# Kernel tuning notes

Measured on AMD Instinct MI355X. Metric: run time of the kernel, lower is better.

Reference implementation:

```python
import jax, jax.numpy as jnp
import numpy as np

N_TOKENS = 4096
EMBED = 2048
D_ATTN = 2048


def setup_inputs() -> dict:
    key = jax.random.key(0)
    k1, k2, k3, k4 = jax.random.split(key, 4)
    # torch.rand -> uniform [0,1); keeps scores positive so the multiplicative
    # -inf mask acts as a clean causal mask (faithful to original behavior).
    token_embeddings = jax.random.uniform(k1, (N_TOKENS, EMBED), dtype=jnp.float32)
    W_Q = jax.random.uniform(k2, (EMBED, D_ATTN), dtype=jnp.float32)
    W_K = jax.random.uniform(k3, (EMBED, D_ATTN), dtype=jnp.float32)
    W_V = jax.random.uniform(k4, (EMBED, D_ATTN), dtype=jnp.float32)
    return {"token_embeddings": token_embeddings, "W_Q": W_Q, "W_K": W_K, "W_V": W_V}


def reference(token_embeddings, W_Q, W_K, W_V):
    n = token_embeddings.shape[0]
    d = W_Q.shape[1]
    # mask: 1 on/below diagonal, -inf strictly above (multiplicative, as in source)
    neg_inf = jnp.float32(-jnp.inf)
    mask = jnp.tril(jnp.ones((n, n), dtype=jnp.float32)) + jnp.triu(
        jnp.full((n, n), neg_inf, dtype=jnp.float32), k=1
    )
    Q = token_embeddings @ W_Q          # (n, d)
    K = token_embeddings @ W_K          # (n, d)
    V = token_embeddings @ W_V          # (n, d)
    scores = (Q @ K.T) * mask           # (n, n); upper tri -> -inf (scores > 0)
    scores = scores / jnp.sqrt(jnp.float32(d))
    attn = jax.nn.softmax(scores, axis=-1)
    return attn @ V                     # (n, d)
```

## Files before the change

### kernel.cpp

```cpp
#include <hip/hip_runtime.h>
#include <hip/hip_bf16.h>
#include <cstdint>
#include <cstddef>
#include <cmath>

#define N_TOK 4096
#define EMB   2048
#define DATT  2048

typedef __attribute__((ext_vector_type(8))) short short8;
typedef __attribute__((ext_vector_type(4))) short shortx4;
typedef __attribute__((ext_vector_type(4))) float f32x4;

#define MFMA(a, b, c) __builtin_amdgcn_mfma_f32_16x16x32_bf16(a, b, c, 0, 0, 0)

__device__ __forceinline__ short f2bs(float f) {
  __hip_bfloat16 h = __float2bfloat16(f);
  return __builtin_bit_cast(short, h);
}
__device__ __forceinline__ float bs2f(short s) {
  return __uint_as_float(((unsigned)(unsigned short)s) << 16);
}
__device__ __forceinline__ float ldin(const void* p, size_t i, int isbf) {
  if (isbf) {
    unsigned short u = ((const unsigned short*)p)[i];
    return __uint_as_float(((unsigned int)u) << 16);
  }
  return ((const float*)p)[i];
}

__device__ __forceinline__ size_t swz(int r, int c, int kdim) {
  return ((size_t)((r >> 7) * (kdim >> 3) + (c >> 3)) << 10) +
         (size_t)((r & 127) << 3) + (c & 7);
}

__device__ __forceinline__ void gl16(const short* g, short* l) {
  __builtin_amdgcn_global_load_lds(
      (const __attribute__((address_space(1))) unsigned int*)(const void*)g,
      (__attribute__((address_space(3))) unsigned int*)(void*)l, 16, 0, 0);
}

template <bool THREE>
__device__ __forceinline__ void gemm_core(const short* Ah, const short* Al,
                                          const short* Bh, const short* Bl,
                                          int chunks, int apan, int bpan,
                                          int kmax, short* lds,
                                          f32x4 acc[4][4]) {
  const int NSL = THREE ? 4 : 2;
  int tid = threadIdx.x;
  int lane = tid & 63;
  int wave = tid >> 6;
  int ln = lane & 15, quad = lane >> 4;
  int wm = (wave >> 1) * 64, wn = (wave & 1) * 64;
  int wofs = wave * 512;

  auto stage = [&](int b, int k0) {
    size_t ao = ((size_t)(apan * chunks + (k0 >> 3))) << 10;
    size_t bo = ((size_t)(bpan * chunks + (k0 >> 3))) << 10;
    short* base = lds + b * NSL * 4096;
    const short* sa = Ah + ao + tid * 8;
    const short* sb = Bh + bo + tid * 8;
    gl16(sa,        base + wofs);
    gl16(sa + 2048, base + wofs + 2048);
    gl16(sb,        base + 4096 + wofs);
    gl16(sb + 2048, base + 4096 + wofs + 2048);
    if (THREE) {
      const short* sal = Al + ao + tid * 8;
      const short* sbl = Bl + bo + tid * 8;
      gl16(sal,        base + 8192 + wofs);
      gl16(sal + 2048, base + 8192 + wofs + 2048);
      gl16(sbl,        base + 12288 + wofs);
      gl16(sbl + 2048, base + 12288 + wofs + 2048);
    }
  };

  stage(0, 0);
  int cur = 0;
  int abase = quad * 1024 + (wm + ln) * 8;
  int bbase = quad * 1024 + (wn + ln) * 8;
  for (int k0 = 0; k0 < kmax; k0 += 32) {
    __syncthreads();
    if (k0 + 32 < kmax) stage(cur ^ 1, k0 + 32);
    const short* B0 = lds + cur * NSL * 4096;
    short8 fah[4], fbh[4];
#pragma unroll
    for (int i = 0; i < 4; ++i) fah[i] = *(const short8*)(B0 + abase + i * 128);
#pragma unroll
    for (int j = 0; j < 4; ++j) fbh[j] = *(const short8*)(B0 + 4096 + bbase + j * 128);
    if (THREE) {
      short8 fal[4], fbl[4];
#pragma unroll
      for (int i = 0; i < 4; ++i) fal[i] = *(const short8*)(B0 + 8192 + abase + i * 128);
#pragma unroll
      for (int j = 0; j < 4; ++j) fbl[j] = *(const short8*)(B0 + 12288 + bbase + j * 128);
#pragma unroll
      for (int j = 0; j < 4; ++j)
#pragma unroll
        for (int i = 0; i < 4; ++i) {
          acc[i][j] = MFMA(fah[i], fbh[j], acc[i][j]);
          acc[i][j] = MFMA(fah[i], fbl[j], acc[i][j]);
          acc[i][j] = MFMA(fal[i], fbh[j], acc[i][j]);
        }
    } else {
#pragma unroll
      for (int j = 0; j < 4; ++j)
#pragma unroll
        for (int i = 0; i < 4; ++i) acc[i][j] = MFMA(fah[i], fbh[j], acc[i][j]);
    }
    cur ^= 1;
  }
}

__global__ void k_sniff(const void* x, int* flag) {
  if (threadIdx.x == 0 && blockIdx.x == 0) {
    const unsigned short* u = (const unsigned short*)x;
    int bf = 1;
    for (int i = 0; i < 256; ++i) {
      unsigned short v = u[i];
      if ((v & 0x8000u) || ((v & 0x7FFFu) >= 0x3F80u)) { bf = 0; break; }
    }
    *flag = bf;
  }
}

__global__ __launch_bounds__(256) void k_xbar(const void* X, float* xbar,
                                              const int* flagp) {
  int isbf = *flagp;
  int e = blockIdx.x * 256 + threadIdx.x;
  float s = 0.f;
  for (int r = 0; r < 256; ++r) s += ldin(X, (size_t)r * EMB + e, isbf);
  xbar[e] = s * (1.f / 256.f);
}

__global__ __launch_bounds__(256) void k_split_x(const void* X, short* Xh, short* Xl,
                                                 const int* flagp) {
  int isbf = *flagp;
  size_t base = ((size_t)blockIdx.x * 256 + threadIdx.x) * 4;
  int r = (int)(base >> 11), c = (int)(base & 2047);
  shortx4 h, l;
#pragma unroll
  for (int u = 0; u < 4; ++u) {
    float x = ldin(X, base + u, isbf);
    short hh = f2bs(x);
    h[u] = hh;
    l[u] = f2bs(x - bs2f(hh));
  }
  size_t o = swz(r, c, EMB);
  *(shortx4*)(Xh + o) = h;
  *(shortx4*)(Xl + o) = l;
}

__global__ __launch_bounds__(256) void k_transpose_split(const void* W, short* Wth,
                                                         short* Wtl, int R, int C,
                                                         const int* flagp, int wlo) {
  __shared__ float T[64][65];
  int isbf = *flagp;
  int r0 = blockIdx.y * 64, c0 = blockIdx.x * 64;
  int tid = threadIdx.x;
#pragma unroll
  for (int it = 0; it < 16; ++it) {
    int idx = tid + it * 256;
    int row = idx >> 6, col = idx & 63;
    T[row][col] = ldin(W, (size_t)(r0 + row) * C + c0 + col, isbf);
  }
  __syncthreads();
#pragma unroll
  for (int it = 0; it < 16; ++it) {
    int idx = tid + it * 256;
    int row = idx >> 6, col = idx & 63;
    float x = T[col][row];
    short h = f2bs(x);
    size_t o = swz(c0 + row, r0 + col, R);
    Wth[o] = h;
    if (wlo) Wtl[o] = f2bs(x - bs2f(h));
  }
}

__global__ __launch_bounds__(256) void k_kbar(const short* Wth, const short* Wtl,
                                              const float* xbar, float* kbar) {
  int d = blockIdx.x;
  float s = 0.f;
  for (int e = threadIdx.x; e < EMB; e += 256) {
    size_t o = swz(d, e, EMB);
    s += xbar[e] * (bs2f(Wth[o]) + bs2f(Wtl[o]));
  }
  __shared__ float red[4];
#pragma unroll
  for (int off = 32; off > 0; off >>= 1) s += __shfl_down(s, off);
  if ((threadIdx.x & 63) == 0) red[threadIdx.x >> 6] = s;
  __syncthreads();
  if (threadIdx.x == 0) kbar[d] = red[0] + red[1] + red[2] + red[3];
}

__global__ __launch_bounds__(256, 2) void k_proj3(const short* Ah, const short* Al,
                                                  const short* Bh, const short* Bl,
                                                  short* Ch, short* Cl,
                                                  const float* bias) {
  __shared__ short lds[2 * 4 * 4096];
  f32x4 acc[4][4] = {};
  int row0 = blockIdx.y * 128, col0 = blockIdx.x * 128;
  gemm_core<true>(Ah, Al, Bh, Bl, EMB >> 3, row0 >> 7, col0 >> 7, EMB, lds, acc);
  int tid = threadIdx.x;
  int wave = tid >> 6, lane = tid & 63;
  int ln = lane & 15, quad = lane >> 4;
  int wm = (wave >> 1) * 64, wn = (wave & 1) * 64;
#pragma unroll
  for (int i = 0; i < 4; ++i)
#pragma unroll
    for (int j = 0; j < 4; ++j)
#pragma unroll
      for (int r = 0; r < 4; ++r) {
        int row = row0 + wm + i * 16 + quad * 4 + r;
        int col = col0 + wn + j * 16 + ln;
        float x = acc[i][j][r];
        if (bias) x -= bias[col];
        short h = f2bs(x);
        size_t o = swz(row, col, DATT);
        Ch[o] = h;
        Cl[o] = f2bs(x - bs2f(h));
      }
}

__global__ __launch_bounds__(256, 2) void k_proj1(const short* Ah, const short* Bh,
                                                  short* Ch) {
  __shared__ short lds[2 * 2 * 4096];
  f32x4 acc[4][4] = {};
  int row0 = blockIdx.y * 128, col0 = blockIdx.x * 128;
  gemm_core<false>(Ah, nullptr, Bh, nullptr, EMB >> 3, row0 >> 7, col0 >> 7, EMB,
                   lds, acc);
  int tid = threadIdx.x;
  int wave = tid >> 6, lane = tid & 63;
  int ln = lane & 15, quad = lane >> 4;
  int wm = (wave >> 1) * 64, wn = (wave & 1) * 64;
#pragma unroll
  for (int i = 0; i < 4; ++i)
#pragma unroll
    for (int j = 0; j < 4; ++j)
#pragma unroll
      for (int r = 0; r < 4; ++r) {
        int row = row0 + wm + i * 16 + quad * 4 + r;
        int col = col0 + wn + j * 16 + ln;
        Ch[swz(row, col, N_TOK)] = f2bs(acc[i][j][r]);
      }
}

__global__ __launch_bounds__(256, 2) void k_score3(const short* Qh, const short* Ql,
                                                   const short* Kh, const short* Kl,
                                                   float* S) {
  int bi = blockIdx.x;
  int by = (int)((sqrtf(8.f * (float)bi + 1.f) - 1.f) * 0.5f);
  while ((by + 1) * (by + 2) / 2 <= bi) ++by;
  while (by * (by + 1) / 2 > bi) --by;
  int bx = bi - by * (by + 1) / 2;
  __shared__ short lds[2 * 4 * 4096];
  f32x4 acc[4][4] = {};
  gemm_core<true>(Qh, Ql, Kh, Kl, DATT >> 3, by, bx, DATT, lds, acc);
  int row0 = by * 128, col0 = bx * 128;
  int tid = threadIdx.x;
  int wave = tid >> 6, lane = tid & 63;
  int ln = lane & 15, quad = lane >> 4;
  int wm = (wave >> 1) * 64, wn = (wave & 1) * 64;
  const float scale = 0.022097086912079608f;
#pragma unroll
  for (int i = 0; i < 4; ++i)
#pragma unroll
    for (int j = 0; j < 4; ++j)
#pragma unroll
      for (int r = 0; r < 4; ++r) {
        int row = row0 + wm + i * 16 + quad * 4 + r;
        int col = col0 + wn + j * 16 + ln;
        if (col <= row) S[(size_t)row * N_TOK + col] = acc[i][j][r] * scale;
      }
}

__global__ __launch_bounds__(256) void k_softmax(const float* S, short* P) {
  int i = blockIdx.x;
  const float* row = S + (size_t)i * N_TOK;
  int len = i + 1;
  int tid = threadIdx.x;
  __shared__ float red[4];
  float m = -3.402823466e38f;
  for (int j = tid; j < len; j += 256) m = fmaxf(m, row[j]);
#pragma unroll
  for (int off = 32; off > 0; off >>= 1) m = fmaxf(m, __shfl_down(m, off));
  if ((tid & 63) == 0) red[tid >> 6] = m;
  __syncthreads();
  m = fmaxf(fmaxf(red[0], red[1]), fmaxf(red[2], red[3]));
  __syncthreads();
  float s = 0.f;
  for (int j = tid; j < len; j += 256) s += __expf(row[j] - m);
#pragma unroll
  for (int off = 32; off > 0; off >>= 1) s += __shfl_down(s, off);
  if ((tid & 63) == 0) red[tid >> 6] = s;
  __syncthreads();
  s = red[0] + red[1] + red[2] + red[3];
  float inv = 1.f / s;
  size_t rbase = ((size_t)(i >> 7) * (N_TOK >> 3) << 10) + (size_t)((i & 127) << 3);
  for (int j = tid; j < len; j += 256)
    P[rbase + ((size_t)(j >> 3) << 10) + (j & 7)] = f2bs(__expf(row[j] - m) * inv);
  for (int j = len + tid; j < N_TOK; j += 256)
    P[rbase + ((size_t)(j >> 3) << 10) + (j & 7)] = 0;
}

__global__ __launch_bounds__(256, 2) void k_out(const short* Ph, const short* Vh,
                                                void* Co, const int* flagp) {
  __shared__ short lds[2 * 2 * 4096];
  f32x4 acc[4][4] = {};
  int row0 = blockIdx.y * 128, col0 = blockIdx.x * 128;
  gemm_core<false>(Ph, nullptr, Vh, nullptr, N_TOK >> 3, row0 >> 7, col0 >> 7,
                   row0 + 128, lds, acc);
  int isbf = *flagp;
  int tid = threadIdx.x;
  int wave = tid >> 6, lane = tid & 63;
  int ln = lane & 15, quad = lane >> 4;
  int wm = (wave >> 1) * 64, wn = (wave & 1) * 64;
#pragma unroll
  for (int i = 0; i < 4; ++i)
#pragma unroll
    for (int j = 0; j < 4; ++j)
#pragma unroll
      for (int r = 0; r < 4; ++r) {
        int row = row0 + wm + i * 16 + quad * 4 + r;
        int col = col0 + wn + j * 16 + ln;
        size_t idx = (size_t)row * DATT + col;
        if (isbf) ((__hip_bfloat16*)Co)[idx] = __float2bfloat16(acc[i][j][r]);
        else      ((float*)Co)[idx] = acc[i][j][r];
      }
}

extern "C" void kernel_launch(void* const* d_in, const int* in_sizes, int n_in,
                              void* d_out, int out_size, void* d_ws, size_t ws_size,
                              hipStream_t stream) {
  const void* X  = d_in[0];
  const void* WQ = d_in[1];
  const void* WK = d_in[2];
  const void* WV = d_in[3];

  float* ws   = (float*)d_ws;
  int*   flag = (int*)d_ws;
  float* xbar = ws + 256;
  float* kbar = ws + 2560;
  short* p0   = (short*)(ws + 16384);
  const size_t M8 = (size_t)N_TOK * DATT;
  const size_t M4 = (size_t)EMB * DATT;
  short* Xh  = p0;
  short* Xl  = Xh + M8;
  short* Wth = Xl + M8;
  short* Wtl = Wth + M4;
  float* S   = (float*)p0;
  short* Qh  = p0 + 4 * M8;
  short* Ql  = Qh + M8;
  short* Kh  = Ql + M8;
  short* Kl  = Kh + M8;
  short* Vt  = Kl + M8;
  short* P   = Qh;

  dim3 blk(256);

  k_sniff<<<1, 64, 0, stream>>>(X, flag);
  k_xbar<<<EMB / 256, blk, 0, stream>>>(X, xbar, flag);
  k_split_x<<<(N_TOK * EMB) / 1024, blk, 0, stream>>>(X, Xh, Xl, flag);

  dim3 gt(DATT / 64, EMB / 64);
  dim3 gq(DATT / 128, N_TOK / 128);
  dim3 gv(N_TOK / 128, DATT / 128);

  k_transpose_split<<<gt, blk, 0, stream>>>(WQ, Wth, Wtl, EMB, DATT, flag, 1);
  k_proj3<<<gq, blk, 0, stream>>>(Xh, Xl, Wth, Wtl, Qh, Ql, nullptr);
  k_transpose_split<<<gt, blk, 0, stream>>>(WK, Wth, Wtl, EMB, DATT, flag, 1);
  k_kbar<<<DATT, blk, 0, stream>>>(Wth, Wtl, xbar, kbar);
  k_proj3<<<gq, blk, 0, stream>>>(Xh, Xl, Wth, Wtl, Kh, Kl, kbar);
  k_transpose_split<<<gt, blk, 0, stream>>>(WV, Wth, nullptr, EMB, DATT, flag, 0);
  k_proj1<<<gv, blk, 0, stream>>>(Wth, Xh, Vt);

  dim3 gs((N_TOK / 128) * (N_TOK / 128 + 1) / 2);
  k_score3<<<gs, blk, 0, stream>>>(Qh, Ql, Kh, Kl, S);

  k_softmax<<<N_TOK, blk, 0, stream>>>(S, P);

  dim3 go(DATT / 128, N_TOK / 128);
  k_out<<<go, blk, 0, stream>>>(P, Vt, d_out, flag);
}
```

Before: 700.1 us.

## Use 256x128 tiles with 512 threads and triple-buffered interleaved prefetch GEMM

Adds a new GEMM core, gemm256, used by the Q/K/V projection and output kernels. Each block now runs 8 waves on a 256x128 output tile, with a three-stage LDS ring filled by direct global-to-LDS loads. Prefetches for the stage two steps ahead are issued between the MFMA sub-blocks, and raised wave priority and explicit waitcnt/barrier scheduling are meant to keep the matrix units busy and hide load latency. In exchange, LDS use per block is much larger (about 147KB for the three-product path), so only one block fits per CU, and the grid has half as many blocks.

```diff
diff --git a/kernel.cpp b/kernel.cpp
--- a/kernel.cpp
+++ b/kernel.cpp
@@ -38,6 +38,180 @@
   __builtin_amdgcn_global_load_lds(
       (const __attribute__((address_space(1))) unsigned int*)(const void*)g,
       (__attribute__((address_space(3))) unsigned int*)(void*)l, 16, 0, 0);
+}
+
+template <bool THREE>
+__device__ __forceinline__ void gemm256(const short* __restrict__ Ah,
+                                        const short* __restrict__ Al,
+                                        const short* __restrict__ Bh,
+                                        const short* __restrict__ Bl,
+                                        int kch, int apan, int bpan, int kmax,
+                                        short* lds, f32x4 acc[4][4]) {
+  const int BUF = THREE ? 24576 : 12288;
+  const int ALS = 8192;
+  const int BHS = THREE ? 16384 : 8192;
+  const int BLS = 20480;
+  int tid = threadIdx.x;
+  int lane = tid & 63, wave = tid >> 6;
+  int ln = lane & 15, quad = lane >> 4;
+  int wm = (wave >> 1) * 64, wn = (wave & 1) * 64;
+  int nt = kmax >> 5;
+  int aoffs = ((wm & 128) ? 4096 : 0) + quad * 1024 + ((wm & 64) + ln) * 8;
+  int boffs = quad * 1024 + (wn + ln) * 8;
+
+  auto stg = [&](const short* g, short* l) {
+    gl16(g + tid * 8, l + wave * 512);
+  };
+  const size_t kstr = (size_t)kch << 10;
+
+  auto stageAll = [&](int b, int s) {
+    short* Pb = lds + b * BUF;
+    size_t a0 = ((size_t)(apan * kch + (s << 2)) << 10);
+    size_t b0 = ((size_t)(bpan * kch + (s << 2)) << 10);
+    stg(Ah + a0, Pb);
+    stg(Ah + a0 + kstr, Pb + 4096);
+    if (THREE) {
+      stg(Al + a0, Pb + ALS);
+      stg(Al + a0 + kstr, Pb + ALS + 4096);
+    }
+    stg(Bh + b0, Pb + BHS);
+    if (THREE) stg(Bl + b0, Pb + BLS);
+  };
+  stageAll(0, 0);
+  stageAll(1, 1);
+
+  int bi = 0;
+  for (int t = 0; t < nt; ++t) {
+    if (t + 1 < nt) {
+      if constexpr (THREE) asm volatile("s_waitcnt vmcnt(6)" ::: "memory");
+      else                 asm volatile("s_waitcnt vmcnt(3)" ::: "memory");
+    } else {
+      asm volatile("s_waitcnt vmcnt(0)" ::: "memory");
+    }
+    __builtin_amdgcn_s_barrier();
+    __builtin_amdgcn_sched_barrier(0);
+
+    short* L = lds + bi * BUF;
+    int pi = bi + 2; if (pi > 2) pi -= 3;
+    short* Pb = lds + pi * BUF;
+    bool pf = (t + 2 < nt);
+    size_t pa0 = ((size_t)(apan * kch + ((t + 2) << 2)) << 10);
+    size_t pb0 = ((size_t)(bpan * kch + ((t + 2) << 2)) << 10);
+
+    short8 bh[4];
+#pragma unroll
+    for (int j = 0; j < 4; ++j)
+      bh[j] = *(const short8*)(L + BHS + boffs + j * 128);
+
+    if constexpr (THREE) {
+      short8 bl[4];
+#pragma unroll
+      for (int j = 0; j < 4; ++j)
+        bl[j] = *(const short8*)(L + BLS + boffs + j * 128);
+      {
+        short8 ah = *(const short8*)(L + aoffs);
+        short8 al = *(const short8*)(L + ALS + aoffs);
+        if (pf) { stg(Ah + pa0, Pb); stg(Ah + pa0 + kstr, Pb + 4096); }
+        __builtin_amdgcn_s_barrier();
+        asm volatile("s_waitcnt lgkmcnt(0)" ::: "memory");
+        __builtin_amdgcn_sched_barrier(0);
+        __builtin_amdgcn_s_setprio(1);
+#pragma unroll
+        for (int j = 0; j < 4; ++j) {
+          acc[0][j] = MFMA(ah, bh[j], acc[0][j]);
+          acc[0][j] = MFMA(ah, bl[j], acc[0][j]);
+          acc[0][j] = MFMA(al, bh[j], acc[0][j]);
+        }
+        __builtin_amdgcn_s_setprio(0);
+        __builtin_amdgcn_s_barrier();
+      }
+      {
+        short8 ah = *(const short8*)(L + aoffs + 128);
+        short8 al = *(const short8*)(L + ALS + aoffs + 128);
+        if (pf) { stg(Al + pa0, Pb + ALS); stg(Al + pa0 + kstr, Pb + ALS + 4096); }
+        __builtin_amdgcn_s_barrier();
+        asm volatile("s_waitcnt lgkmcnt(0)" ::: "memory");
+        __builtin_amdgcn_sched_barrier(0);
+        __builtin_amdgcn_s_setprio(1);
+#pragma unroll
+        for (int j = 0; j < 4; ++j) {
+          acc[1][j] = MFMA(ah, bh[j], acc[1][j]);
+          acc[1][j] = MFMA(ah, bl[j], acc[1][j]);
+          acc[1][j] = MFMA(al, bh[j], acc[1][j]);
+        }
+        __builtin_amdgcn_s_setprio(0);
+        __builtin_amdgcn_s_barrier();
+      }
+      {
+        short8 ah = *(const short8*)(L + aoffs + 256);
+        short8 al = *(const short8*)(L + ALS + aoffs + 256);
+        if (pf) stg(Bh + pb0, Pb + BHS);
+        __builtin_amdgcn_s_barrier();
+        asm volatile("s_waitcnt lgkmcnt(0)" ::: "memory");
+        __builtin_amdgcn_sched_barrier(0);
+        __builtin_amdgcn_s_setprio(1);
+#pragma unroll
+        for (int j = 0; j < 4; ++j) {
+          acc[2][j] = MFMA(ah, bh[j], acc[2][j]);
+          acc[2][j] = MFMA(ah, bl[j], acc[2][j]);
+          acc[2][j] = MFMA(al, bh[j], acc[2][j]);
+        }
+        __builtin_amdgcn_s_setprio(0);
+        __builtin_amdgcn_s_barrier();
+      }
+      {
+        short8 ah = *(const short8*)(L + aoffs + 384);
+        short8 al = *(const short8*)(L + ALS + aoffs + 384);
+        if (pf) stg(Bl + pb0, Pb + BLS);
+        __builtin_amdgcn_s_barrier();
+        asm volatile("s_waitcnt lgkmcnt(0)" ::: "memory");
+        __builtin_amdgcn_sched_barrier(0);
+        __builtin_amdgcn_s_setprio(1);
+#pragma unroll
+        for (int j = 0; j < 4; ++j) {
+          acc[3][j] = MFMA(ah, bh[j], acc[3][j]);
+          acc[3][j] = MFMA(ah, bl[j], acc[3][j]);
+          acc[3][j] = MFMA(al, bh[j], acc[3][j]);
+        }
+        __builtin_amdgcn_s_setprio(0);
+        __builtin_amdgcn_s_barrier();
+      }
+    } else {
+      {
+        short8 a0 = *(const short8*)(L + aoffs);
+        short8 a1 = *(const short8*)(L + aoffs + 128);
+        if (pf) { stg(Ah + pa0, Pb); stg(Ah + pa0 + kstr, Pb + 4096); }
+        __builtin_amdgcn_s_barrier();
+        asm volatile("s_waitcnt lgkmcnt(0)" ::: "memory");
+        __builtin_amdgcn_sched_barrier(0);
+        __builtin_amdgcn_s_setprio(1);
+#pragma unroll
+        for (int j = 0; j < 4; ++j) {
+          acc[0][j] = MFMA(a0, bh[j], acc[0][j]);
+          acc[1][j] = MFMA(a1, bh[j], acc[1][j]);
+        }
+        __builtin_amdgcn_s_setprio(0);
+        __builtin_amdgcn_s_barrier();
+      }
+      {
+        short8 a2 = *(const short8*)(L + aoffs + 256);
+        short8 a3 = *(const short8*)(L + aoffs + 384);
+        if (pf) stg(Bh + pb0, Pb + BHS);
+        __builtin_amdgcn_s_barrier();
+        asm volatile("s_waitcnt lgkmcnt(0)" ::: "memory");
+        __builtin_amdgcn_sched_barrier(0);
+        __builtin_amdgcn_s_setprio(1);
+#pragma unroll
+        for (int j = 0; j < 4; ++j) {
+          acc[2][j] = MFMA(a2, bh[j], acc[2][j]);
+          acc[3][j] = MFMA(a3, bh[j], acc[3][j]);
+        }
+        __builtin_amdgcn_s_setprio(0);
+        __builtin_amdgcn_s_barrier();
+      }
+    }
+    ++bi; if (bi > 2) bi = 0;
+  }
 }
 
 template <bool THREE>
@@ -192,14 +366,14 @@
   if (threadIdx.x == 0) kbar[d] = red[0] + red[1] + red[2] + red[3];
 }
 
-__global__ __launch_bounds__(256, 2) void k_proj3(const short* Ah, const short* Al,
-                                                  const short* Bh, const short* Bl,
-                                                  short* Ch, short* Cl,
-                                                  const float* bias) {
-  __shared__ short lds[2 * 4 * 4096];
+__global__ __launch_bounds__(512) void k_proj3(const short* Ah, const short* Al,
+                                               const short* Bh, const short* Bl,
+                                               short* Ch, short* Cl,
+                                               const float* bias) {
+  __shared__ short lds[3 * 24576];
   f32x4 acc[4][4] = {};
-  int row0 = blockIdx.y * 128, col0 = blockIdx.x * 128;
-  gemm_core<true>(Ah, Al, Bh, Bl, EMB >> 3, row0 >> 7, col0 >> 7, EMB, lds, acc);
+  int row0 = blockIdx.y * 256, col0 = blockIdx.x * 128;
+  gemm256<true>(Ah, Al, Bh, Bl, EMB >> 3, row0 >> 7, col0 >> 7, EMB, lds, acc);
   int tid = threadIdx.x;
   int wave = tid >> 6, lane = tid & 63;
   int ln = lane & 15, quad = lane >> 4;
@@ -221,13 +395,13 @@
       }
 }
 
-__global__ __launch_bounds__(256, 2) void k_proj1(const short* Ah, const short* Bh,
-                                                  short* Ch) {
-  __shared__ short lds[2 * 2 * 4096];
+__global__ __launch_bounds__(512) void k_proj1(const short* Ah, const short* Bh,
+                                               short* Ch) {
+  __shared__ short lds[3 * 12288];
   f32x4 acc[4][4] = {};
-  int row0 = blockIdx.y * 128, col0 = blockIdx.x * 128;
-  gemm_core<false>(Ah, nullptr, Bh, nullptr, EMB >> 3, row0 >> 7, col0 >> 7, EMB,
-                   lds, acc);
+  int row0 = blockIdx.y * 256, col0 = blockIdx.x * 128;
+  gemm256<false>(Ah, nullptr, Bh, nullptr, EMB >> 3, row0 >> 7, col0 >> 7, EMB,
+                 lds, acc);
   int tid = threadIdx.x;
   int wave = tid >> 6, lane = tid & 63;
   int ln = lane & 15, quad = lane >> 4;
@@ -302,13 +476,13 @@
     P[rbase + ((size_t)(j >> 3) << 10) + (j & 7)] = 0;
 }
 
-__global__ __launch_bounds__(256, 2) void k_out(const short* Ph, const short* Vh,
-                                                void* Co, const int* flagp) {
-  __shared__ short lds[2 * 2 * 4096];
+__global__ __launch_bounds__(512) void k_out(const short* Ph, const short* Vh,
+                                             void* Co, const int* flagp) {
+  __shared__ short lds[3 * 12288];
   f32x4 acc[4][4] = {};
-  int row0 = blockIdx.y * 128, col0 = blockIdx.x * 128;
-  gemm_core<false>(Ph, nullptr, Vh, nullptr, N_TOK >> 3, row0 >> 7, col0 >> 7,
-                   row0 + 128, lds, acc);
+  int row0 = blockIdx.y * 256, col0 = blockIdx.x * 128;
+  gemm256<false>(Ph, nullptr, Vh, nullptr, N_TOK >> 3, row0 >> 7, col0 >> 7,
+                 row0 + 256, lds, acc);
   int isbf = *flagp;
   int tid = threadIdx.x;
   int wave = tid >> 6, lane = tid & 63;
@@ -356,28 +530,29 @@
   short* P   = Qh;
 
   dim3 blk(256);
+  dim3 blk512(512);
 
   k_sniff<<<1, 64, 0, stream>>>(X, flag);
   k_xbar<<<EMB / 256, blk, 0, stream>>>(X, xbar, flag);
   k_split_x<<<(N_TOK * EMB) / 1024, blk, 0, stream>>>(X, Xh, Xl, flag);
 
   dim3 gt(DATT / 64, EMB / 64);
-  dim3 gq(DATT / 128, N_TOK / 128);
-  dim3 gv(N_TOK / 128, DATT / 128);
+  dim3 gq(DATT / 128, N_TOK / 256);
+  dim3 gv(N_TOK / 128, DATT / 256);
 
   k_transpose_split<<<gt, blk, 0, stream>>>(WQ, Wth, Wtl, EMB, DATT, flag, 1);
-  k_proj3<<<gq, blk, 0, stream>>>(Xh, Xl, Wth, Wtl, Qh, Ql, nullptr);
+  k_proj3<<<gq, blk512, 0, stream>>>(Xh, Xl, Wth, Wtl, Qh, Ql, nullptr);
   k_transpose_split<<<gt, blk, 0, stream>>>(WK, Wth, Wtl, EMB, DATT, flag, 1);
   k_kbar<<<DATT, blk, 0, stream>>>(Wth, Wtl, xbar, kbar);
-  k_proj3<<<gq, blk, 0, stream>>>(Xh, Xl, Wth, Wtl, Kh, Kl, kbar);
+  k_proj3<<<gq, blk512, 0, stream>>>(Xh, Xl, Wth, Wtl, Kh, Kl, kbar);
   k_transpose_split<<<gt, blk, 0, stream>>>(WV, Wth, nullptr, EMB, DATT, flag, 0);
-  k_proj1<<<gv, blk, 0, stream>>>(Wth, Xh, Vt);
+  k_proj1<<<gv, blk512, 0, stream>>>(Wth, Xh, Vt);
 
   dim3 gs((N_TOK / 128) * (N_TOK / 128 + 1) / 2);
   k_score3<<<gs, blk, 0, stream>>>(Qh, Ql, Kh, Kl, S);
 
   k_softmax<<<N_TOK, blk, 0, stream>>>(S, P);
 
-  dim3 go(DATT / 128, N_TOK / 128);
-  k_out<<<go, blk, 0, stream>>>(P, Vt, d_out, flag);
-}
+  dim3 go(DATT / 128, N_TOK / 256);
+  k_out<<<go, blk512, 0, stream>>>(P, Vt, d_out, flag);
+}
```

Measured after the change: 683.0 us. 2.4% less time.

## Prefetch two K-tiles ahead with explicit vmcnt waits and MFMA priority

Applied to the files above, without the earlier changes.

Rewrites the shared GEMM mainloop so it prefetches two tiles ahead instead of one. Each step waits with a partial s_waitcnt vmcnt so only the current tile's loads must land, and barriers sit on both sides of compute. MFMA sections run at raised wave priority via s_setprio. The output GEMM also launches its longest causal row blocks first to reduce tail imbalance. The hand-written vmcnt counts are fragile if the compiler emits other vector memory ops in the loop.

```diff
diff --git a/kernel.cpp b/kernel.cpp
--- a/kernel.cpp
+++ b/kernel.cpp
@@ -41,58 +41,64 @@
 }
 
 template <bool THREE>
-__device__ __forceinline__ void gemm_core(const short* Ah, const short* Al,
-                                          const short* Bh, const short* Bl,
-                                          int chunks, int apan, int bpan,
-                                          int kmax, short* lds,
-                                          f32x4 acc[4][4]) {
-  const int NSL = THREE ? 4 : 2;
-  int tid = threadIdx.x;
-  int lane = tid & 63;
-  int wave = tid >> 6;
+__device__ __forceinline__ void gemmP(const short* __restrict__ Ah,
+                                      const short* __restrict__ Al,
+                                      const short* __restrict__ Bh,
+                                      const short* __restrict__ Bl,
+                                      int chunks, int apan, int bpan,
+                                      int kmax, short* lds, f32x4 acc[4][4]) {
+  const int BUF = THREE ? 16384 : 8192;
+  int tid = threadIdx.x;
+  int lane = tid & 63, wave = tid >> 6;
   int ln = lane & 15, quad = lane >> 4;
   int wm = (wave >> 1) * 64, wn = (wave & 1) * 64;
   int wofs = wave * 512;
-
-  auto stage = [&](int b, int k0) {
-    size_t ao = ((size_t)(apan * chunks + (k0 >> 3))) << 10;
-    size_t bo = ((size_t)(bpan * chunks + (k0 >> 3))) << 10;
-    short* base = lds + b * NSL * 4096;
-    const short* sa = Ah + ao + tid * 8;
-    const short* sb = Bh + bo + tid * 8;
-    gl16(sa,        base + wofs);
-    gl16(sa + 2048, base + wofs + 2048);
-    gl16(sb,        base + 4096 + wofs);
-    gl16(sb + 2048, base + 4096 + wofs + 2048);
+  int nt = kmax >> 5;
+
+  auto stage = [&](int b, int t) {
+    size_t ao = ((size_t)(apan * chunks + (t << 2))) << 10;
+    size_t bo = ((size_t)(bpan * chunks + (t << 2))) << 10;
+    short* base = lds + b * BUF;
+    gl16(Ah + ao + tid * 8,        base + wofs);
+    gl16(Ah + ao + 2048 + tid * 8, base + wofs + 2048);
+    gl16(Bh + bo + tid * 8,        base + 4096 + wofs);
+    gl16(Bh + bo + 2048 + tid * 8, base + 4096 + wofs + 2048);
     if (THREE) {
-      const short* sal = Al + ao + tid * 8;
-      const short* sbl = Bl + bo + tid * 8;
-      gl16(sal,        base + 8192 + wofs);
-      gl16(sal + 2048, base + 8192 + wofs + 2048);
-      gl16(sbl,        base + 12288 + wofs);
-      gl16(sbl + 2048, base + 12288 + wofs + 2048);
+      gl16(Al + ao + tid * 8,        base + 8192 + wofs);
+      gl16(Al + ao + 2048 + tid * 8, base + 8192 + wofs + 2048);
+      gl16(Bl + bo + tid * 8,        base + 12288 + wofs);
+      gl16(Bl + bo + 2048 + tid * 8, base + 12288 + wofs + 2048);
     }
   };
-
   stage(0, 0);
-  int cur = 0;
+  if (nt > 1) stage(1, 1);
+
   int abase = quad * 1024 + (wm + ln) * 8;
   int bbase = quad * 1024 + (wn + ln) * 8;
-  for (int k0 = 0; k0 < kmax; k0 += 32) {
-    __syncthreads();
-    if (k0 + 32 < kmax) stage(cur ^ 1, k0 + 32);
-    const short* B0 = lds + cur * NSL * 4096;
+  for (int t = 0; t < nt; ++t) {
+    int cur = t & 1;
+    if (t + 1 < nt) {
+      if constexpr (THREE) asm volatile("s_waitcnt vmcnt(8)" ::: "memory");
+      else                 asm volatile("s_waitcnt vmcnt(4)" ::: "memory");
+    } else {
+      asm volatile("s_waitcnt vmcnt(0)" ::: "memory");
+    }
+    __builtin_amdgcn_s_barrier();
+    __builtin_amdgcn_sched_barrier(0);
+
+    const short* L = lds + cur * BUF;
     short8 fah[4], fbh[4];
 #pragma unroll
-    for (int i = 0; i < 4; ++i) fah[i] = *(const short8*)(B0 + abase + i * 128);
-#pragma unroll
-    for (int j = 0; j < 4; ++j) fbh[j] = *(const short8*)(B0 + 4096 + bbase + j * 128);
-    if (THREE) {
+    for (int i = 0; i < 4; ++i) fah[i] = *(const short8*)(L + abase + i * 128);
+#pragma unroll
+    for (int j = 0; j < 4; ++j) fbh[j] = *(const short8*)(L + 4096 + bbase + j * 128);
+    if constexpr (THREE) {
       short8 fal[4], fbl[4];
 #pragma unroll
-      for (int i = 0; i < 4; ++i) fal[i] = *(const short8*)(B0 + 8192 + abase + i * 128);
-#pragma unroll
-      for (int j = 0; j < 4; ++j) fbl[j] = *(const short8*)(B0 + 12288 + bbase + j * 128);
+      for (int i = 0; i < 4; ++i) fal[i] = *(const short8*)(L + 8192 + abase + i * 128);
+#pragma unroll
+      for (int j = 0; j < 4; ++j) fbl[j] = *(const short8*)(L + 12288 + bbase + j * 128);
+      __builtin_amdgcn_s_setprio(1);
 #pragma unroll
       for (int j = 0; j < 4; ++j)
 #pragma unroll
@@ -101,13 +107,18 @@
           acc[i][j] = MFMA(fah[i], fbl[j], acc[i][j]);
           acc[i][j] = MFMA(fal[i], fbh[j], acc[i][j]);
         }
+      __builtin_amdgcn_s_setprio(0);
     } else {
+      __builtin_amdgcn_s_setprio(1);
 #pragma unroll
       for (int j = 0; j < 4; ++j)
 #pragma unroll
         for (int i = 0; i < 4; ++i) acc[i][j] = MFMA(fah[i], fbh[j], acc[i][j]);
+      __builtin_amdgcn_s_setprio(0);
     }
-    cur ^= 1;
+    __builtin_amdgcn_sched_barrier(0);
+    __builtin_amdgcn_s_barrier();
+    if (t + 2 < nt) stage(cur, t + 2);
   }
 }
 
@@ -196,10 +207,10 @@
                                                   const short* Bh, const short* Bl,
                                                   short* Ch, short* Cl,
                                                   const float* bias) {
-  __shared__ short lds[2 * 4 * 4096];
+  __shared__ short lds[2 * 16384];
   f32x4 acc[4][4] = {};
   int row0 = blockIdx.y * 128, col0 = blockIdx.x * 128;
-  gemm_core<true>(Ah, Al, Bh, Bl, EMB >> 3, row0 >> 7, col0 >> 7, EMB, lds, acc);
+  gemmP<true>(Ah, Al, Bh, Bl, EMB >> 3, row0 >> 7, col0 >> 7, EMB, lds, acc);
   int tid = threadIdx.x;
   int wave = tid >> 6, lane = tid & 63;
   int ln = lane & 15, quad = lane >> 4;
@@ -223,11 +234,11 @@
 
 __global__ __launch_bounds__(256, 2) void k_proj1(const short* Ah, const short* Bh,
                                                   short* Ch) {
-  __shared__ short lds[2 * 2 * 4096];
+  __shared__ short lds[2 * 8192];
   f32x4 acc[4][4] = {};
   int row0 = blockIdx.y * 128, col0 = blockIdx.x * 128;
-  gemm_core<false>(Ah, nullptr, Bh, nullptr, EMB >> 3, row0 >> 7, col0 >> 7, EMB,
-                   lds, acc);
+  gemmP<false>(Ah, nullptr, Bh, nullptr, EMB >> 3, row0 >> 7, col0 >> 7, EMB,
+               lds, acc);
   int tid = threadIdx.x;
   int wave = tid >> 6, lane = tid & 63;
   int ln = lane & 15, quad = lane >> 4;
@@ -252,9 +263,9 @@
   while ((by + 1) * (by + 2) / 2 <= bi) ++by;
   while (by * (by + 1) / 2 > bi) --by;
   int bx = bi - by * (by + 1) / 2;
-  __shared__ short lds[2 * 4 * 4096];
+  __shared__ short lds[2 * 16384];
   f32x4 acc[4][4] = {};
-  gemm_core<true>(Qh, Ql, Kh, Kl, DATT >> 3, by, bx, DATT, lds, acc);
+  gemmP<true>(Qh, Ql, Kh, Kl, DATT >> 3, by, bx, DATT, lds, acc);
   int row0 = by * 128, col0 = bx * 128;
   int tid = threadIdx.x;
   int wave = tid >> 6, lane = tid & 63;
@@ -304,11 +315,11 @@
 
 __global__ __launch_bounds__(256, 2) void k_out(const short* Ph, const short* Vh,
                                                 void* Co, const int* flagp) {
-  __shared__ short lds[2 * 2 * 4096];
+  __shared__ short lds[2 * 8192];
   f32x4 acc[4][4] = {};
-  int row0 = blockIdx.y * 128, col0 = blockIdx.x * 128;
-  gemm_core<false>(Ph, nullptr, Vh, nullptr, N_TOK >> 3, row0 >> 7, col0 >> 7,
-                   row0 + 128, lds, acc);
+  int row0 = (gridDim.y - 1 - blockIdx.y) * 128, col0 = blockIdx.x * 128;
+  gemmP<false>(Ph, nullptr, Vh, nullptr, N_TOK >> 3, row0 >> 7, col0 >> 7,
+               row0 + 128, lds, acc);
   int isbf = *flagp;
   int tid = threadIdx.x;
   int wave = tid >> 6, lane = tid & 63;
```

Measured after the change: 671.6 us. -4.1%, faster.

## Add triple-buffered single-precision GEMM core and XCD-aware block remapping

Applied to the files above, without the earlier changes.

Adds a new GEMM core that keeps three LDS stages with waitcnt-based prefetch two tiles ahead. k_proj1 and k_out now use it and get a 3-blocks-per-CU launch bound. All GEMM kernels switch to 1D grids with a remap that interleaves blocks across the 8 XCDs for better L2 locality. k_out also orders its causal bands so that long and short rows are mixed for load balance. The cost is more LDS per block and more complex index arithmetic.

```diff
diff --git a/kernel.cpp b/kernel.cpp
--- a/kernel.cpp
+++ b/kernel.cpp
@@ -111,6 +111,53 @@
   }
 }
 
+__device__ __forceinline__ void gemm1d2(const short* __restrict__ Ah,
+                                        const short* __restrict__ Bh,
+                                        int chunks, int apan, int bpan,
+                                        int kmax, short* lds, f32x4 acc[4][4]) {
+  int tid = threadIdx.x;
+  int lane = tid & 63, wave = tid >> 6;
+  int ln = lane & 15, quad = lane >> 4;
+  int wm = (wave >> 1) * 64, wn = (wave & 1) * 64;
+  int wofs = wave * 512;
+  int nt = kmax >> 5;
+
+  auto stage = [&](int b, int t) {
+    size_t ao = ((size_t)(apan * chunks + (t << 2))) << 10;
+    size_t bo = ((size_t)(bpan * chunks + (t << 2))) << 10;
+    short* base = lds + b * 8192;
+    gl16(Ah + ao + tid * 8,        base + wofs);
+    gl16(Ah + ao + 2048 + tid * 8, base + wofs + 2048);
+    gl16(Bh + bo + tid * 8,        base + 4096 + wofs);
+    gl16(Bh + bo + 2048 + tid * 8, base + 4096 + wofs + 2048);
+  };
+  stage(0, 0);
+  if (nt > 1) stage(1, 1);
+
+  int abase = quad * 1024 + (wm + ln) * 8;
+  int bbase = quad * 1024 + (wn + ln) * 8;
+  int bi = 0;
+  for (int t = 0; t < nt; ++t) {
+    if (t + 1 < nt) asm volatile("s_waitcnt vmcnt(4)" ::: "memory");
+    else            asm volatile("s_waitcnt vmcnt(0)" ::: "memory");
+    __builtin_amdgcn_s_barrier();
+    __builtin_amdgcn_sched_barrier(0);
+    int pi = bi + 2; if (pi > 2) pi -= 3;
+    if (t + 2 < nt) stage(pi, t + 2);
+    const short* L = lds + bi * 8192;
+    short8 fah[4], fbh[4];
+#pragma unroll
+    for (int i = 0; i < 4; ++i) fah[i] = *(const short8*)(L + abase + i * 128);
+#pragma unroll
+    for (int j = 0; j < 4; ++j) fbh[j] = *(const short8*)(L + 4096 + bbase + j * 128);
+#pragma unroll
+    for (int j = 0; j < 4; ++j)
+#pragma unroll
+      for (int i = 0; i < 4; ++i) acc[i][j] = MFMA(fah[i], fbh[j], acc[i][j]);
+    ++bi; if (bi > 2) bi = 0;
+  }
+}
+
 __global__ void k_sniff(const void* x, int* flag) {
   if (threadIdx.x == 0 && blockIdx.x == 0) {
     const unsigned short* u = (const unsigned short*)x;
@@ -196,9 +243,11 @@
                                                   const short* Bh, const short* Bl,
                                                   short* Ch, short* Cl,
                                                   const float* bias) {
-  __shared__ short lds[2 * 4 * 4096];
+  __shared__ short lds[2 * 16384];
+  int bid = blockIdx.x;
+  int s = ((bid & 7) << 6) | (bid >> 3);
+  int row0 = (s >> 4) << 7, col0 = (s & 15) << 7;
   f32x4 acc[4][4] = {};
-  int row0 = blockIdx.y * 128, col0 = blockIdx.x * 128;
   gemm_core<true>(Ah, Al, Bh, Bl, EMB >> 3, row0 >> 7, col0 >> 7, EMB, lds, acc);
   int tid = threadIdx.x;
   int wave = tid >> 6, lane = tid & 63;
@@ -221,13 +270,14 @@
       }
 }
 
-__global__ __launch_bounds__(256, 2) void k_proj1(const short* Ah, const short* Bh,
+__global__ __launch_bounds__(256, 3) void k_proj1(const short* Ah, const short* Bh,
                                                   short* Ch) {
-  __shared__ short lds[2 * 2 * 4096];
+  __shared__ short lds[3 * 8192];
+  int bid = blockIdx.x;
+  int s = ((bid & 7) << 6) | (bid >> 3);
+  int row0 = (s >> 5) << 7, col0 = (s & 31) << 7;
   f32x4 acc[4][4] = {};
-  int row0 = blockIdx.y * 128, col0 = blockIdx.x * 128;
-  gemm_core<false>(Ah, nullptr, Bh, nullptr, EMB >> 3, row0 >> 7, col0 >> 7, EMB,
-                   lds, acc);
+  gemm1d2(Ah, Bh, EMB >> 3, row0 >> 7, col0 >> 7, EMB, lds, acc);
   int tid = threadIdx.x;
   int wave = tid >> 6, lane = tid & 63;
   int ln = lane & 15, quad = lane >> 4;
@@ -247,12 +297,13 @@
 __global__ __launch_bounds__(256, 2) void k_score3(const short* Qh, const short* Ql,
                                                    const short* Kh, const short* Kl,
                                                    float* S) {
-  int bi = blockIdx.x;
+  int bi0 = blockIdx.x;
+  int bi = (bi0 & 7) * 66 + (bi0 >> 3);
   int by = (int)((sqrtf(8.f * (float)bi + 1.f) - 1.f) * 0.5f);
   while ((by + 1) * (by + 2) / 2 <= bi) ++by;
   while (by * (by + 1) / 2 > bi) --by;
   int bx = bi - by * (by + 1) / 2;
-  __shared__ short lds[2 * 4 * 4096];
+  __shared__ short lds[2 * 16384];
   f32x4 acc[4][4] = {};
   gemm_core<true>(Qh, Ql, Kh, Kl, DATT >> 3, by, bx, DATT, lds, acc);
   int row0 = by * 128, col0 = bx * 128;
@@ -302,13 +353,18 @@
     P[rbase + ((size_t)(j >> 3) << 10) + (j & 7)] = 0;
 }
 
-__global__ __launch_bounds__(256, 2) void k_out(const short* Ph, const short* Vh,
+__global__ __launch_bounds__(256, 3) void k_out(const short* Ph, const short* Vh,
                                                 void* Co, const int* flagp) {
-  __shared__ short lds[2 * 2 * 4096];
+  __shared__ short lds[3 * 8192];
+  int bid = blockIdx.x;
+  int half = bid >> 8;
+  int r = bid & 255;
+  int s = ((r & 7) << 5) | (r >> 3);
+  int bb = s >> 4;
+  int band = half ? bb : (31 - bb);
+  int row0 = band << 7, col0 = (s & 15) << 7;
   f32x4 acc[4][4] = {};
-  int row0 = blockIdx.y * 128, col0 = blockIdx.x * 128;
-  gemm_core<false>(Ph, nullptr, Vh, nullptr, N_TOK >> 3, row0 >> 7, col0 >> 7,
-                   row0 + 128, lds, acc);
+  gemm1d2(Ph, Vh, N_TOK >> 3, row0 >> 7, col0 >> 7, row0 + 128, lds, acc);
   int isbf = *flagp;
   int tid = threadIdx.x;
   int wave = tid >> 6, lane = tid & 63;
@@ -319,12 +375,12 @@
 #pragma unroll
     for (int j = 0; j < 4; ++j)
 #pragma unroll
-      for (int r = 0; r < 4; ++r) {
-        int row = row0 + wm + i * 16 + quad * 4 + r;
+      for (int r2 = 0; r2 < 4; ++r2) {
+        int row = row0 + wm + i * 16 + quad * 4 + r2;
         int col = col0 + wn + j * 16 + ln;
         size_t idx = (size_t)row * DATT + col;
-        if (isbf) ((__hip_bfloat16*)Co)[idx] = __float2bfloat16(acc[i][j][r]);
-        else      ((float*)Co)[idx] = acc[i][j][r];
+        if (isbf) ((__hip_bfloat16*)Co)[idx] = __float2bfloat16(acc[i][j][r2]);
+        else      ((float*)Co)[idx] = acc[i][j][r2];
       }
 }
 
@@ -362,22 +418,18 @@
   k_split_x<<<(N_TOK * EMB) / 1024, blk, 0, stream>>>(X, Xh, Xl, flag);
 
   dim3 gt(DATT / 64, EMB / 64);
-  dim3 gq(DATT / 128, N_TOK / 128);
-  dim3 gv(N_TOK / 128, DATT / 128);
 
   k_transpose_split<<<gt, blk, 0, stream>>>(WQ, Wth, Wtl, EMB, DATT, flag, 1);
-  k_proj3<<<gq, blk, 0, stream>>>(Xh, Xl, Wth, Wtl, Qh, Ql, nullptr);
+  k_proj3<<<dim3(512), blk, 0, stream>>>(Xh, Xl, Wth, Wtl, Qh, Ql, nullptr);
   k_transpose_split<<<gt, blk, 0, stream>>>(WK, Wth, Wtl, EMB, DATT, flag, 1);
   k_kbar<<<DATT, blk, 0, stream>>>(Wth, Wtl, xbar, kbar);
-  k_proj3<<<gq, blk, 0, stream>>>(Xh, Xl, Wth, Wtl, Kh, Kl, kbar);
+  k_proj3<<<dim3(512), blk, 0, stream>>>(Xh, Xl, Wth, Wtl, Kh, Kl, kbar);
   k_transpose_split<<<gt, blk, 0, stream>>>(WV, Wth, nullptr, EMB, DATT, flag, 0);
-  k_proj1<<<gv, blk, 0, stream>>>(Wth, Xh, Vt);
-
-  dim3 gs((N_TOK / 128) * (N_TOK / 128 + 1) / 2);
-  k_score3<<<gs, blk, 0, stream>>>(Qh, Ql, Kh, Kl, S);
+  k_proj1<<<dim3(512), blk, 0, stream>>>(Wth, Xh, Vt);
+
+  k_score3<<<dim3(528), blk, 0, stream>>>(Qh, Ql, Kh, Kl, S);
 
   k_softmax<<<N_TOK, blk, 0, stream>>>(S, P);
 
-  dim3 go(DATT / 128, N_TOK / 128);
-  k_out<<<go, blk, 0, stream>>>(P, Vt, d_out, flag);
-}
+  k_out<<<dim3(512), blk, 0, stream>>>(P, Vt, d_out, flag);
+}
```

After: 660.0 us. -5.7%, faster.
